# Kernel optimization log

Hardware: AMD Instinct MI355X
Metric: run time of the kernel (lower is better)

The kernel has to match this reference:

```python
import jax, jax.numpy as jnp
import numpy as np

N, E, EMB, H, DH, FF, L = 2500, 10000, 32, 4, 8, 32, 1
EPS = 1e-5


def setup_inputs() -> dict:
    key = jax.random.key(0)
    ks = jax.random.split(key, 20)
    rn = lambda k, shape, s=0.1: jax.random.normal(k, shape, jnp.float32) * s
    return {
        'feat': rn(ks[0], (N, EMB), 1.0),
        'query': rn(ks[1], (E, L, H, DH)),
        'src_key_w': rn(ks[2], (E, L, H, FF, EMB)),
        'dst_key_w': rn(ks[3], (E, L, H, FF, EMB)),
        'src_key_b': rn(ks[4], (E, L, H, FF)),
        'dst_key_b': rn(ks[5], (E, L, H, FF)),
        'edge_key_w': rn(ks[6], (E, L, H, FF, DH)),
        'edge_key_b': rn(ks[7], (E, L, H, DH)),
        'src_val_w': rn(ks[8], (E, L, H, FF, EMB)),
        'dst_val_w': rn(ks[9], (E, L, H, FF, EMB)),
        'src_val_b': rn(ks[10], (E, L, H, FF)),
        'dst_val_b': rn(ks[11], (E, L, H, FF)),
        'edge_val_w': rn(ks[12], (E, L, H, FF, DH)),
        'edge_val_b': rn(ks[13], (E, L, H, DH)),
        'key_gamma': jnp.ones((DH,), jnp.float32),
        'key_beta': jnp.zeros((DH,), jnp.float32),
        'val_gamma': jnp.ones((DH,), jnp.float32),
        'val_beta': jnp.zeros((DH,), jnp.float32),
        'out_gamma': jnp.ones((DH,), jnp.float32),
        'out_beta': jnp.zeros((DH,), jnp.float32),
        'src': jax.random.randint(ks[14], (E,), 0, N, jnp.int32),
        'dst': jax.random.randint(ks[15], (E,), 0, N, jnp.int32),
        'i': 0,
    }


def _ln(x, g, b):
    m = x.mean(-1, keepdims=True)
    v = x.var(-1, keepdims=True)
    return (x - m) * jax.lax.rsqrt(v + EPS) * g + b


def _ffn(fs, fd, uw, vw, ub, vb, ew, eb, g, b):
    # per-edge, per-head two-layer feedforward with distinct weights
    # fs, fd: (E, EMB); uw/vw: (E,H,FF,EMB); ew: (E,H,FF,DH)
    h = (jnp.einsum('ehfd,ed->ehf', uw, fs) + ub
         + jnp.einsum('ehfd,ed->ehf', vw, fd) + vb)
    h = jax.nn.relu(h)
    o = jnp.einsum('ehfk,ehf->ehk', ew, h) + eb  # (E,H,DH)
    return _ln(o, g, b)


def reference(feat, query, src_key_w, dst_key_w, src_key_b, dst_key_b,
              edge_key_w, edge_key_b, src_val_w, dst_val_w, src_val_b,
              dst_val_b, edge_val_w, edge_val_b, key_gamma, key_beta,
              val_gamma, val_beta, out_gamma, out_beta, src, dst, i):
    n = feat.shape[0]
    fs, fd = feat[src], feat[dst]
    k = _ffn(fs, fd, src_key_w[:, i], dst_key_w[:, i], src_key_b[:, i],
             dst_key_b[:, i], edge_key_w[:, i], edge_key_b[:, i],
             key_gamma, key_beta)
    logits = (k * query[:, i]).sum(-1)  # (E,H)
    # edge softmax grouped by destination node
    m = jax.ops.segment_max(logits, dst, num_segments=n)
    ex = jnp.exp(logits - m[dst])
    s = jax.ops.segment_sum(ex, dst, num_segments=n)
    attn = ex / s[dst]  # (E,H)
    v = _ffn(fs, fd, src_val_w[:, i], dst_val_w[:, i], src_val_b[:, i],
             dst_val_b[:, i], edge_val_w[:, i], edge_val_b[:, i],
             val_gamma, val_beta)
    msg = v * attn[..., None]  # (E,H,DH)
    agg = jax.ops.segment_sum(msg, dst, num_segments=n)  # (N,H,DH)
    out = _ln(agg, out_gamma, out_beta)
    return out.reshape(feat.shape), attn
```

## Files before the change

kernel.cpp:

```cpp
#include <hip/hip_runtime.h>

#define NN   2500
#define NE   10000
#define EMBD 32
#define NH   4
#define DHD  8
#define FFD  32
#define EPSC 1e-5f

typedef float vf4 __attribute__((ext_vector_type(4)));

__device__ __forceinline__ float dot4v(vf4 a, vf4 b) {
    return a.x * b.x + a.y * b.y + a.z * b.z + a.w * b.w;
}

__device__ __forceinline__ vf4 ffn_compute(
    const vf4* fs, const vf4* fd,
    const vf4* u, const vf4* v,
    vf4 w2, float b1, vf4 b2,
    vf4 g4, vf4 bt4)
{
    float p = dot4v(u[0], fs[0]) + dot4v(u[1], fs[1])
            + dot4v(u[2], fs[2]) + dot4v(u[3], fs[3])
            + dot4v(v[0], fd[0]) + dot4v(v[1], fd[1])
            + dot4v(v[2], fd[2]) + dot4v(v[3], fd[3]);
    p += __shfl_xor(p, 1);
    float hv = fmaxf(p + b1, 0.0f);

    vf4 o = w2 * hv;
    #pragma unroll
    for (int m = 2; m <= 32; m <<= 1) {
        o.x += __shfl_xor(o.x, m);
        o.y += __shfl_xor(o.y, m);
        o.z += __shfl_xor(o.z, m);
        o.w += __shfl_xor(o.w, m);
    }
    o += b2;

    float s1 = o.x + o.y + o.z + o.w;
    float s2 = o.x * o.x + o.y * o.y + o.z * o.z + o.w * o.w;
    s1 += __shfl_xor(s1, 1);
    s2 += __shfl_xor(s2, 1);
    float mean = s1 * 0.125f;
    float var  = s2 * 0.125f - mean * mean;
    float rs   = rsqrtf(var + EPSC);
    return (o - mean) * rs * g4 + bt4;
}

__global__ __launch_bounds__(256, 2) void edge_kernel(
    const float* __restrict__ feat, const float* __restrict__ query,
    const float* __restrict__ skw, const float* __restrict__ dkw,
    const float* __restrict__ skb, const float* __restrict__ dkb,
    const float* __restrict__ ekw, const float* __restrict__ ekb,
    const float* __restrict__ svw, const float* __restrict__ dvw,
    const float* __restrict__ svb, const float* __restrict__ dvb,
    const float* __restrict__ evw, const float* __restrict__ evb,
    const float* __restrict__ kg, const float* __restrict__ kbeta,
    const float* __restrict__ vg, const float* __restrict__ vbeta,
    const int* __restrict__ src, const int* __restrict__ dst,
    float* __restrict__ s_den, float* __restrict__ ex_out,
    float* __restrict__ v_out)
{
    int gid = blockIdx.x * 256 + threadIdx.x;
    int wid = gid >> 6;
    if (wid >= NE * NH) return;
    int lane = threadIdx.x & 63;
    int e    = wid >> 2;
    int hh   = wid & 3;
    int half = lane & 1;
    int f2   = lane >> 1;
    int sn = src[e], dn = dst[e];
    size_t eh = (size_t)wid;

    const vf4* ku_p = (const vf4*)(skw + eh * 1024 + lane * 16);
    const vf4* kv_p = (const vf4*)(dkw + eh * 1024 + lane * 16);
    vf4 ku[4], kv[4];
    #pragma unroll
    for (int j = 0; j < 4; j++) ku[j] = ku_p[j];
    #pragma unroll
    for (int j = 0; j < 4; j++) kv[j] = kv_p[j];
    vf4 kw2 = *(const vf4*)(ekw + eh * 256 + f2 * DHD + half * 4);
    float kb1 = skb[eh * 32 + f2] + dkb[eh * 32 + f2];
    vf4 kb2 = *(const vf4*)(ekb + eh * 8 + half * 4);
    vf4 q4  = *(const vf4*)(query + eh * 8 + half * 4);
    vf4 kgam = *(const vf4*)(kg    + half * 4);
    vf4 kbet = *(const vf4*)(kbeta + half * 4);

    const vf4* fsp = (const vf4*)(feat + sn * EMBD + half * 16);
    const vf4* fdp = (const vf4*)(feat + dn * EMBD + half * 16);
    vf4 fsr[4], fdr[4];
    #pragma unroll
    for (int j = 0; j < 4; j++) { fsr[j] = fsp[j]; fdr[j] = fdp[j]; }

    const vf4* vu_p = (const vf4*)(svw + eh * 1024 + lane * 16);
    const vf4* vv_p = (const vf4*)(dvw + eh * 1024 + lane * 16);
    vf4 vu[4], vv[4];
    #pragma unroll
    for (int j = 0; j < 4; j++) vu[j] = vu_p[j];
    #pragma unroll
    for (int j = 0; j < 4; j++) vv[j] = vv_p[j];
    vf4 vw2 = *(const vf4*)(evw + eh * 256 + f2 * DHD + half * 4);
    float vb1 = svb[eh * 32 + f2] + dvb[eh * 32 + f2];
    vf4 vb2 = *(const vf4*)(evb + eh * 8 + half * 4);
    vf4 vgam = *(const vf4*)(vg    + half * 4);
    vf4 vbet = *(const vf4*)(vbeta + half * 4);

    __builtin_amdgcn_sched_barrier(0);
    asm volatile("" ::
        "v"(ku[0]), "v"(ku[1]), "v"(ku[2]), "v"(ku[3]),
        "v"(kv[0]), "v"(kv[1]), "v"(kv[2]), "v"(kv[3]),
        "v"(kw2), "v"(kb2), "v"(q4), "v"(kgam), "v"(kbet), "v"(kb1));
    asm volatile("" ::
        "v"(fsr[0]), "v"(fsr[1]), "v"(fsr[2]), "v"(fsr[3]),
        "v"(fdr[0]), "v"(fdr[1]), "v"(fdr[2]), "v"(fdr[3]));
    asm volatile("" ::
        "v"(vu[0]), "v"(vu[1]), "v"(vu[2]), "v"(vu[3]),
        "v"(vv[0]), "v"(vv[1]), "v"(vv[2]), "v"(vv[3]),
        "v"(vw2), "v"(vb2), "v"(vgam), "v"(vbet), "v"(vb1));
    __builtin_amdgcn_sched_barrier(0);

    vf4 kn = ffn_compute(fsr, fdr, ku, kv, kw2, kb1, kb2, kgam, kbet);
    float lp = dot4v(kn, q4);
    lp += __shfl_xor(lp, 1);

    vf4 vn = ffn_compute(fsr, fdr, vu, vv, vw2, vb1, vb2, vgam, vbet);

    if (lane < 2)
        *(vf4*)(v_out + eh * 8 + half * 4) = vn;
    if (lane == 0) {
        float exv = expf(lp);
        ex_out[eh] = exv;
        atomicAdd(s_den + dn * NH + hh, exv);
    }
}

__global__ void zero_kernel(float* __restrict__ p, int n) {
    int i = blockIdx.x * blockDim.x + threadIdx.x;
    if (i < n) p[i] = 0.0f;
}

__global__ void attn_agg_kernel(
    const int* __restrict__ dst, const float* __restrict__ ex,
    const float* __restrict__ s_den, const float* __restrict__ v,
    float* __restrict__ agg, float* __restrict__ attn_out)
{
    int tid = blockIdx.x * blockDim.x + threadIdx.x;
    if (tid >= NE * NH * DHD) return;
    int eh = tid >> 3;
    int dd = tid & 7;
    int e  = eh >> 2;
    int h  = eh & 3;
    int dn = dst[e];
    float a = ex[eh] / s_den[dn * NH + h];
    if (dd == 0) attn_out[eh] = a;
    atomicAdd(agg + (dn * NH + h) * DHD + dd, v[tid] * a);
}

__global__ void out_ln_kernel(
    const float* __restrict__ agg, const float* __restrict__ g,
    const float* __restrict__ b, float* __restrict__ out)
{
    int tid = blockIdx.x * blockDim.x + threadIdx.x;
    if (tid >= NN * NH) return;
    vf4 a0 = *(const vf4*)(agg + tid * 8);
    vf4 a1 = *(const vf4*)(agg + tid * 8 + 4);
    float s1 = a0.x + a0.y + a0.z + a0.w + a1.x + a1.y + a1.z + a1.w;
    float s2 = a0.x * a0.x + a0.y * a0.y + a0.z * a0.z + a0.w * a0.w
             + a1.x * a1.x + a1.y * a1.y + a1.z * a1.z + a1.w * a1.w;
    float mean = s1 * 0.125f;
    float var  = s2 * 0.125f - mean * mean;
    float rs   = rsqrtf(var + EPSC);
    vf4 g0 = *(const vf4*)(g);
    vf4 g1 = *(const vf4*)(g + 4);
    vf4 b0 = *(const vf4*)(b);
    vf4 b1 = *(const vf4*)(b + 4);
    *(vf4*)(out + tid * 8)     = (a0 - mean) * rs * g0 + b0;
    *(vf4*)(out + tid * 8 + 4) = (a1 - mean) * rs * g1 + b1;
}

extern "C" void kernel_launch(void* const* d_in, const int* in_sizes, int n_in,
                              void* d_out, int out_size, void* d_ws, size_t ws_size,
                              hipStream_t stream) {
    const float* feat  = (const float*)d_in[0];
    const float* query = (const float*)d_in[1];
    const float* skw   = (const float*)d_in[2];
    const float* dkw   = (const float*)d_in[3];
    const float* skb   = (const float*)d_in[4];
    const float* dkb   = (const float*)d_in[5];
    const float* ekw   = (const float*)d_in[6];
    const float* ekb   = (const float*)d_in[7];
    const float* svw   = (const float*)d_in[8];
    const float* dvw   = (const float*)d_in[9];
    const float* svb   = (const float*)d_in[10];
    const float* dvb   = (const float*)d_in[11];
    const float* evw   = (const float*)d_in[12];
    const float* evb   = (const float*)d_in[13];
    const float* kg    = (const float*)d_in[14];
    const float* kbeta = (const float*)d_in[15];
    const float* vg    = (const float*)d_in[16];
    const float* vbeta = (const float*)d_in[17];
    const float* og    = (const float*)d_in[18];
    const float* obeta = (const float*)d_in[19];
    const int*   src   = (const int*)d_in[20];
    const int*   dst   = (const int*)d_in[21];

    float* ws    = (float*)d_ws;
    float* s_den = ws;
    float* agg   = ws + 10000;
    float* ex    = ws + 90000;
    float* vbuf  = ws + 130000;

    float* out  = (float*)d_out;

    zero_kernel<<<(90000 + 255) / 256, 256, 0, stream>>>(ws, 90000);

    edge_kernel<<<(NE * NH * 64) / 256, 256, 0, stream>>>(
        feat, query, skw, dkw, skb, dkb, ekw, ekb,
        svw, dvw, svb, dvb, evw, evb,
        kg, kbeta, vg, vbeta, src, dst,
        s_den, ex, vbuf);

    attn_agg_kernel<<<(NE * NH * DHD + 255) / 256, 256, 0, stream>>>(
        dst, ex, s_den, vbuf, agg, out + NN * EMBD);

    out_ln_kernel<<<(NN * NH + 255) / 256, 256, 0, stream>>>(
        agg, og, obeta, out);
}
```

Baseline: 141.2 us.

## Coalesce per-edge weight loads with lane-strided vf4 indexing and shuffle redistribution

Each lane of the edge kernel now loads vf4 elements at stride 64 (j*64+lane) from the weight matrices, so each wave's loads are fully contiguous. Previously each lane read 16 consecutive floats. Because the lane-to-data mapping changes, the first-layer dot products are now reduced across groups of 8 lanes and redistributed with __shfl so each lane gets its hidden unit. Bias, gamma and beta loads are moved after the scheduling barrier to cut live registers, and occupancy is raised to 3 blocks per SM. The cost is extra shuffle and select work per FFN.

```diff
diff --git a/kernel.cpp b/kernel.cpp
--- a/kernel.cpp
+++ b/kernel.cpp
@@ -15,25 +15,32 @@
 }
 
 __device__ __forceinline__ vf4 ffn_compute(
-    const vf4* fs, const vf4* fd,
-    const vf4* u, const vf4* v,
-    vf4 w2, float b1, vf4 b2,
-    vf4 g4, vf4 bt4)
-{
-    float p = dot4v(u[0], fs[0]) + dot4v(u[1], fs[1])
-            + dot4v(u[2], fs[2]) + dot4v(u[3], fs[3])
-            + dot4v(v[0], fd[0]) + dot4v(v[1], fd[1])
-            + dot4v(v[2], fd[2]) + dot4v(v[3], fd[3]);
-    p += __shfl_xor(p, 1);
-    float hv = fmaxf(p + b1, 0.0f);
-
-    vf4 o = w2 * hv;
+    const vf4* U, const vf4* V, vf4 E, vf4 FS, vf4 FD,
+    float b1, vf4 b2, vf4 g4, vf4 bt4, int lane)
+{
+    float p0 = dot4v(U[0], FS) + dot4v(V[0], FD);
+    float p1 = dot4v(U[1], FS) + dot4v(V[1], FD);
+    float p2 = dot4v(U[2], FS) + dot4v(V[2], FD);
+    float p3 = dot4v(U[3], FS) + dot4v(V[3], FD);
+    #pragma unroll
+    for (int m = 1; m <= 4; m <<= 1) {
+        p0 += __shfl_xor(p0, m); p1 += __shfl_xor(p1, m);
+        p2 += __shfl_xor(p2, m); p3 += __shfl_xor(p3, m);
+    }
+
+    int f = lane >> 1;
+    int s = ((f & 7) << 3) | (lane & 7);
+    float h0 = __shfl(p0, s), h1 = __shfl(p1, s);
+    float h2 = __shfl(p2, s), h3 = __shfl(p3, s);
+    int j = lane >> 4;
+    float hp = (j == 0) ? h0 : (j == 1) ? h1 : (j == 2) ? h2 : h3;
+    float h  = fmaxf(hp + b1, 0.0f);
+
+    vf4 o = E * h;
     #pragma unroll
     for (int m = 2; m <= 32; m <<= 1) {
-        o.x += __shfl_xor(o.x, m);
-        o.y += __shfl_xor(o.y, m);
-        o.z += __shfl_xor(o.z, m);
-        o.w += __shfl_xor(o.w, m);
+        o.x += __shfl_xor(o.x, m); o.y += __shfl_xor(o.y, m);
+        o.z += __shfl_xor(o.z, m); o.w += __shfl_xor(o.w, m);
     }
     o += b2;
 
@@ -47,7 +54,7 @@
     return (o - mean) * rs * g4 + bt4;
 }
 
-__global__ __launch_bounds__(256, 2) void edge_kernel(
+__global__ __launch_bounds__(256, 3) void edge_kernel(
     const float* __restrict__ feat, const float* __restrict__ query,
     const float* __restrict__ skw, const float* __restrict__ dkw,
     const float* __restrict__ skb, const float* __restrict__ dkb,
@@ -67,63 +74,54 @@
     int lane = threadIdx.x & 63;
     int e    = wid >> 2;
     int hh   = wid & 3;
+    int c    = lane & 7;
+    int f    = lane >> 1;
     int half = lane & 1;
-    int f2   = lane >> 1;
     int sn = src[e], dn = dst[e];
     size_t eh = (size_t)wid;
 
-    const vf4* ku_p = (const vf4*)(skw + eh * 1024 + lane * 16);
-    const vf4* kv_p = (const vf4*)(dkw + eh * 1024 + lane * 16);
-    vf4 ku[4], kv[4];
-    #pragma unroll
-    for (int j = 0; j < 4; j++) ku[j] = ku_p[j];
-    #pragma unroll
-    for (int j = 0; j < 4; j++) kv[j] = kv_p[j];
-    vf4 kw2 = *(const vf4*)(ekw + eh * 256 + f2 * DHD + half * 4);
-    float kb1 = skb[eh * 32 + f2] + dkb[eh * 32 + f2];
-    vf4 kb2 = *(const vf4*)(ekb + eh * 8 + half * 4);
-    vf4 q4  = *(const vf4*)(query + eh * 8 + half * 4);
-    vf4 kgam = *(const vf4*)(kg    + half * 4);
-    vf4 kbet = *(const vf4*)(kbeta + half * 4);
-
-    const vf4* fsp = (const vf4*)(feat + sn * EMBD + half * 16);
-    const vf4* fdp = (const vf4*)(feat + dn * EMBD + half * 16);
-    vf4 fsr[4], fdr[4];
-    #pragma unroll
-    for (int j = 0; j < 4; j++) { fsr[j] = fsp[j]; fdr[j] = fdp[j]; }
-
-    const vf4* vu_p = (const vf4*)(svw + eh * 1024 + lane * 16);
-    const vf4* vv_p = (const vf4*)(dvw + eh * 1024 + lane * 16);
-    vf4 vu[4], vv[4];
-    #pragma unroll
-    for (int j = 0; j < 4; j++) vu[j] = vu_p[j];
-    #pragma unroll
-    for (int j = 0; j < 4; j++) vv[j] = vv_p[j];
-    vf4 vw2 = *(const vf4*)(evw + eh * 256 + f2 * DHD + half * 4);
-    float vb1 = svb[eh * 32 + f2] + dvb[eh * 32 + f2];
-    vf4 vb2 = *(const vf4*)(evb + eh * 8 + half * 4);
-    vf4 vgam = *(const vf4*)(vg    + half * 4);
-    vf4 vbet = *(const vf4*)(vbeta + half * 4);
+    const vf4* ku_p = (const vf4*)(skw + eh * 1024);
+    const vf4* kv_p = (const vf4*)(dkw + eh * 1024);
+    const vf4* vu_p = (const vf4*)(svw + eh * 1024);
+    const vf4* vv_p = (const vf4*)(dvw + eh * 1024);
+    vf4 KU[4], KV[4], VU[4], VV[4];
+    #pragma unroll
+    for (int j = 0; j < 4; j++) KU[j] = ku_p[j * 64 + lane];
+    #pragma unroll
+    for (int j = 0; j < 4; j++) KV[j] = kv_p[j * 64 + lane];
+    #pragma unroll
+    for (int j = 0; j < 4; j++) VU[j] = vu_p[j * 64 + lane];
+    #pragma unroll
+    for (int j = 0; j < 4; j++) VV[j] = vv_p[j * 64 + lane];
+    vf4 KE = ((const vf4*)(ekw + eh * 256))[lane];
+    vf4 VE = ((const vf4*)(evw + eh * 256))[lane];
+    vf4 FS = ((const vf4*)(feat + sn * EMBD))[c];
+    vf4 FD = ((const vf4*)(feat + dn * EMBD))[c];
+    vf4 q4 = ((const vf4*)(query + eh * 8))[half];
 
     __builtin_amdgcn_sched_barrier(0);
     asm volatile("" ::
-        "v"(ku[0]), "v"(ku[1]), "v"(ku[2]), "v"(ku[3]),
-        "v"(kv[0]), "v"(kv[1]), "v"(kv[2]), "v"(kv[3]),
-        "v"(kw2), "v"(kb2), "v"(q4), "v"(kgam), "v"(kbet), "v"(kb1));
+        "v"(KU[0]), "v"(KU[1]), "v"(KU[2]), "v"(KU[3]),
+        "v"(KV[0]), "v"(KV[1]), "v"(KV[2]), "v"(KV[3]),
+        "v"(KE), "v"(FS), "v"(FD), "v"(q4));
     asm volatile("" ::
-        "v"(fsr[0]), "v"(fsr[1]), "v"(fsr[2]), "v"(fsr[3]),
-        "v"(fdr[0]), "v"(fdr[1]), "v"(fdr[2]), "v"(fdr[3]));
-    asm volatile("" ::
-        "v"(vu[0]), "v"(vu[1]), "v"(vu[2]), "v"(vu[3]),
-        "v"(vv[0]), "v"(vv[1]), "v"(vv[2]), "v"(vv[3]),
-        "v"(vw2), "v"(vb2), "v"(vgam), "v"(vbet), "v"(vb1));
+        "v"(VU[0]), "v"(VU[1]), "v"(VU[2]), "v"(VU[3]),
+        "v"(VV[0]), "v"(VV[1]), "v"(VV[2]), "v"(VV[3]),
+        "v"(VE));
     __builtin_amdgcn_sched_barrier(0);
 
-    vf4 kn = ffn_compute(fsr, fdr, ku, kv, kw2, kb1, kb2, kgam, kbet);
+    float kb1 = skb[eh * 32 + f] + dkb[eh * 32 + f];
+    float vb1 = svb[eh * 32 + f] + dvb[eh * 32 + f];
+    vf4 kb2 = ((const vf4*)(ekb + eh * 8))[half];
+    vf4 vb2 = ((const vf4*)(evb + eh * 8))[half];
+    vf4 kgam = ((const vf4*)kg)[half],   kbet = ((const vf4*)kbeta)[half];
+    vf4 vgam = ((const vf4*)vg)[half],   vbet = ((const vf4*)vbeta)[half];
+
+    vf4 kn = ffn_compute(KU, KV, KE, FS, FD, kb1, kb2, kgam, kbet, lane);
     float lp = dot4v(kn, q4);
     lp += __shfl_xor(lp, 1);
 
-    vf4 vn = ffn_compute(fsr, fdr, vu, vv, vw2, vb1, vb2, vgam, vbet);
+    vf4 vn = ffn_compute(VU, VV, VE, FS, FD, vb1, vb2, vgam, vbet, lane);
 
     if (lane < 2)
         *(vf4*)(v_out + eh * 8 + half * 4) = vn;
```

After: 143.7 us. Within noise of the previous version (+1.7%).
